# Optimization experiments

Hardware: AMD Instinct MI355X
Metric: run time of the kernel (lower is better)

The kernel has to match this reference:

```python
import jax, jax.numpy as jnp
import numpy as np

N = 4096            # tokens (dim 0 of x)
LATENT = 1024       # latent_vector_size
H = 16              # num_heads
DK = 64             # key_dim
DV = 64             # val_dim
MHK = H * DK        # 1024, width of q and k blocks


def setup_inputs() -> dict:
    key = jax.random.key(0)
    ks = jax.random.split(key, 5)
    return {
        "x": jax.random.normal(ks[0], (N, LATENT), dtype=jnp.float32),
        "w_qkv": jax.random.normal(ks[1], (LATENT, H * (2 * DK + DV)), dtype=jnp.float32) * (1.0 / np.sqrt(LATENT)),
        "b_qkv": jax.random.normal(ks[2], (H * (2 * DK + DV),), dtype=jnp.float32) * 0.01,
        "w_out": jax.random.normal(ks[3], (H * DV, LATENT), dtype=jnp.float32) * (1.0 / np.sqrt(H * DV)),
        "b_out": jax.random.normal(ks[4], (LATENT,), dtype=jnp.float32) * 0.01,
    }


def reference(x, w_qkv, b_qkv, w_out, b_out):
    # qkv projection: [N, H*(2*Dk+Dv)]
    qkv = x @ w_qkv + b_qkv
    # NOTE: the original module does NOT split into heads; q/k/v are the
    # concatenated head dims and a single [N, N] score matrix is formed,
    # scaled by sqrt(key_dim) (per-head dim), not sqrt(H*key_dim).
    q = qkv[:, :MHK]                 # [N, H*Dk]
    k = qkv[:, MHK:2 * MHK]          # [N, H*Dk]
    v = qkv[:, 2 * MHK:]             # [N, H*Dv]
    scores = (q @ k.T) * (1.0 / jnp.sqrt(jnp.float32(DK)))  # [N, N]
    attn = jax.nn.softmax(scores, axis=-1)
    out = attn @ v                   # [N, H*Dv]
    return out @ w_out + b_out       # [N, LATENT]
```

## Files before the change

### kernel.cpp

```cpp
#include <hip/hip_runtime.h>
#include <hip/hip_fp16.h>


typedef _Float16 half_t;
typedef _Float16 half8 __attribute__((ext_vector_type(8)));
typedef _Float16 half4 __attribute__((ext_vector_type(4)));
typedef float f32x4 __attribute__((ext_vector_type(4)));

static constexpr int N_TOK = 4096;
static constexpr int LATENT = 1024;
static constexpr int QKVN = 3072;

#define DEVI __device__ __forceinline__
#define BAR() __builtin_amdgcn_s_barrier()
#define PRIO(x) __builtin_amdgcn_s_setprio(x)
#define VMCNT(n) asm volatile("s_waitcnt vmcnt(" #n ")" ::: "memory")

DEVI void gld_lds16(const half_t* g, half_t* l) {
  __builtin_amdgcn_global_load_lds(
      (const __attribute__((address_space(1))) void*)g,
      (__attribute__((address_space(3))) void*)l,
      16, 0, 0);
}

DEVI f32x4 MFMA(half8 a, half8 b, f32x4 c) {
  return __builtin_amdgcn_mfma_f32_16x16x32_f16(a, b, c, 0, 0, 0);
}


DEVI void stageH(const half_t* __restrict__ g, int ld, half_t* lbase, int tid) {
#pragma unroll
  for (int i = 0; i < 2; ++i) {
    int c = tid + i * 512;
    int r = c >> 2;
    int k8 = ((c & 3) ^ ((r >> 1) & 3)) * 8;
    gld_lds16(g + (size_t)r * ld + k8, lbase + c * 8);
  }
}

template <int MODE>
__launch_bounds__(512, 2)
__global__ void gemm8h(const half_t* __restrict__ A, int lda,
                       const half_t* __restrict__ B, int ldb,
                       void* __restrict__ Cout, int ldc,
                       const float* __restrict__ bias, int K) {
  __shared__ half_t Alds[2][2][256 * 32];
  __shared__ half_t Blds[2][2][256 * 32];

  const int tid = threadIdx.x;
  const int lane = tid & 63;
  const int wid = tid >> 6;

  const int nx = gridDim.x;
  const int nwg = nx * gridDim.y;
  const int bid = blockIdx.y * nx + blockIdx.x;
  const int cpx = nwg >> 3;
  const int swz = (bid & 7) * cpx + (bid >> 3);
  const int rowBlk = (swz / nx) * 256;
  const int colBlk = (swz % nx) * 256;

  const int wr = (wid >> 2) * 128;
  const int wc = (wid & 3) * 64;
  const int fr = lane & 15;
  const int fs = lane >> 4;

  const int kOff = blockIdx.z * K;
  const half_t* Ag = A + (size_t)rowBlk * lda + kOff;
  const half_t* Bg = B + (size_t)colBlk * ldb + kOff;

  f32x4 acc[8][4] = {};
  const int NT = K >> 6;

  stageH(Ag, lda, Alds[0][0], tid);
  stageH(Bg, ldb, Blds[0][0], tid);
  stageH(Ag + 32, lda, Alds[0][1], tid);
  stageH(Bg + 32, ldb, Blds[0][1], tid);
  VMCNT(4);
  BAR();

  for (int kt = 0; kt < NT; ++kt) {
    const int b = kt & 1;
    const bool st = (kt + 1 < NT);
    const half_t* AgN = Ag + (kt + 1) * 64;
    const half_t* BgN = Bg + (kt + 1) * 64;

    half8 af[8], bf[4];
#pragma unroll
    for (int kh = 0; kh < 2; ++kh) {
      const half_t* Ac = Alds[b][kh];
      const half_t* Bc = Blds[b][kh];
#pragma unroll
      for (int m = 0; m < 8; ++m) {
        int row = wr + m * 16 + fr;
        af[m] = *(const half8*)(Ac + row * 32 + ((fs ^ ((row >> 1) & 3)) * 8));
      }
#pragma unroll
      for (int n = 0; n < 4; ++n) {
        int row = wc + n * 16 + fr;
        bf[n] = *(const half8*)(Bc + row * 32 + ((fs ^ ((row >> 1) & 3)) * 8));
      }
      if (st) {
        stageH(AgN + kh * 32, lda, Alds[b ^ 1][kh], tid);
        stageH(BgN + kh * 32, ldb, Blds[b ^ 1][kh], tid);
      }
      BAR();
      PRIO(1);
#pragma unroll
      for (int m = 0; m < 8; ++m)
#pragma unroll
        for (int n = 0; n < 4; ++n)
          acc[m][n] = MFMA(af[m], bf[n], acc[m][n]);
      PRIO(0);
      if (st) VMCNT(4);
      else if (kh == 0) VMCNT(0);
      BAR();
    }
  }

  const size_t zoff = (MODE == 2) ? (size_t)blockIdx.z * N_TOK * ldc : 0;
#pragma unroll
  for (int m = 0; m < 8; ++m) {
#pragma unroll
    for (int n = 0; n < 4; ++n) {
#pragma unroll
      for (int j = 0; j < 4; ++j) {
        int row = rowBlk + wr + m * 16 + (lane >> 4) * 4 + j;
        int col = colBlk + wc + n * 16 + fr;
        float v = acc[m][n][j];
        if (MODE == 0) {
          v += bias[col];
          if (col < 1024) v *= 0.125f;
          ((half_t*)Cout)[(size_t)row * ldc + col] = (half_t)v;
        } else if (MODE == 1) {
          ((half_t*)Cout)[(size_t)row * ldc + col] = (half_t)v;
        } else {
          ((half_t*)Cout)[zoff + (size_t)row * ldc + col] = (half_t)v;
        }
      }
    }
  }
}

DEVI void stage32p(const half_t* __restrict__ g, int ld, half_t* lbase, int tid) {
#pragma unroll
  for (int c = tid; c < 128 * 4; c += 256) {
    int r = c >> 2;
    int k8 = ((c & 3) ^ ((r >> 1) & 3)) * 8;
    gld_lds16(g + (size_t)r * ld + k8, lbase + c * 8);
  }
}

__launch_bounds__(256, 2)
__global__ void vwt_softmax(const half_t* __restrict__ wo,
                            const half_t* __restrict__ v,
                            half_t* __restrict__ vwT,
                            const half_t* __restrict__ S,
                            half_t* __restrict__ P) {
  __shared__ __align__(16) char smem[32768];
  const int bid = blockIdx.x;
  const int tid = threadIdx.x;

  if (bid < 256) {
    constexpr int BM = 128, BN = 128, MF = 4, NF = 4;
    half_t* At = (half_t*)smem;
    half_t* Bt = At + 2 * BM * 32;

    const int lane = tid & 63;
    const int wid = tid >> 6;
    const int swz = (bid & 7) * 32 + (bid >> 3);
    const int rowBlk = (swz >> 5) * BM;
    const int colBlk = (swz & 31) * BN;

    const int wr = (wid >> 1) * (BM / 2);
    const int wc = (wid & 1) * (BN / 2);
    const int fr = lane & 15;
    const int fs = lane >> 4;

    const half_t* Ag = wo + (size_t)rowBlk * LATENT;
    const half_t* Bg = v + (size_t)colBlk * QKVN;

    f32x4 acc[MF][NF] = {};
    const int NT = LATENT >> 5;
    stage32p(Ag, LATENT, At, tid);
    stage32p(Bg, QKVN, Bt, tid);
    __syncthreads();

    int cur = 0;
    for (int t = 0; t < NT; ++t) {
      if (t + 1 < NT) {
        stage32p(Ag + (t + 1) * 32, LATENT, At + (cur ^ 1) * BM * 32, tid);
        stage32p(Bg + (t + 1) * 32, QKVN, Bt + (cur ^ 1) * BN * 32, tid);
      }
      const half_t* Ac = At + cur * BM * 32;
      const half_t* Bc = Bt + cur * BN * 32;
      half8 af[MF], bf[NF];
#pragma unroll
      for (int m = 0; m < MF; ++m) {
        int row = wr + m * 16 + fr;
        af[m] = *(const half8*)(Ac + row * 32 + ((fs ^ ((row >> 1) & 3)) * 8));
      }
#pragma unroll
      for (int n = 0; n < NF; ++n) {
        int row = wc + n * 16 + fr;
        bf[n] = *(const half8*)(Bc + row * 32 + ((fs ^ ((row >> 1) & 3)) * 8));
      }
#pragma unroll
      for (int m = 0; m < MF; ++m)
#pragma unroll
        for (int n = 0; n < NF; ++n)
          acc[m][n] = MFMA(af[m], bf[n], acc[m][n]);
      __syncthreads();
      cur ^= 1;
    }

#pragma unroll
    for (int m = 0; m < MF; ++m)
#pragma unroll
      for (int n = 0; n < NF; ++n)
#pragma unroll
        for (int j = 0; j < 4; ++j) {
          int row = rowBlk + wr + m * 16 + (lane >> 4) * 4 + j;
          int col = colBlk + wc + n * 16 + fr;
          vwT[(size_t)row * N_TOK + col] = (half_t)acc[m][n][j];
        }
  } else {
    const int row = bid - 256;
    float* redm = (float*)smem;
    float* reds = redm + 4;
    const half8* s8 = (const half8*)(S + (size_t)row * N_TOK);

    half8 vv[2];
    float lmax = -1e30f;
#pragma unroll
    for (int i = 0; i < 2; ++i) {
      vv[i] = s8[tid + i * 256];
#pragma unroll
      for (int j = 0; j < 8; ++j) lmax = fmaxf(lmax, (float)vv[i][j]);
    }
#pragma unroll
    for (int off = 32; off; off >>= 1) lmax = fmaxf(lmax, __shfl_xor(lmax, off));
    if ((tid & 63) == 0) redm[tid >> 6] = lmax;
    __syncthreads();
    lmax = fmaxf(fmaxf(redm[0], redm[1]), fmaxf(redm[2], redm[3]));

    float e[16];
    float lsum = 0.f;
#pragma unroll
    for (int i = 0; i < 2; ++i)
#pragma unroll
      for (int j = 0; j < 8; ++j) {
        float ev = __expf((float)vv[i][j] - lmax);
        e[i * 8 + j] = ev;
        lsum += ev;
      }
#pragma unroll
    for (int off = 32; off; off >>= 1) lsum += __shfl_xor(lsum, off);
    if ((tid & 63) == 0) reds[tid >> 6] = lsum;
    __syncthreads();
    float inv = 1.f / (reds[0] + reds[1] + reds[2] + reds[3]);

    half8* p8 = (half8*)(P + (size_t)row * N_TOK);
#pragma unroll
    for (int i = 0; i < 2; ++i) {
      half8 h;
#pragma unroll
      for (int j = 0; j < 8; ++j) h[j] = (half_t)(e[i * 8 + j] * inv);
      p8[tid + i * 256] = h;
    }
  }
}

__launch_bounds__(256)
__global__ void reduce_bias4(const half_t* __restrict__ p, const float* __restrict__ bias,
                             float* __restrict__ out) {
  int i = blockIdx.x * 256 + threadIdx.x;
  const size_t stride8 = (size_t)N_TOK * LATENT / 8;
  half8 a = ((const half8*)p)[i];
  half8 b = ((const half8*)p)[i + stride8];
  half8 c = ((const half8*)p)[i + 2 * stride8];
  half8 d = ((const half8*)p)[i + 3 * stride8];
  float4 e0 = ((const float4*)bias)[(i & 127) * 2];
  float4 e1 = ((const float4*)bias)[(i & 127) * 2 + 1];
  float r[8];
#pragma unroll
  for (int j = 0; j < 8; ++j)
    r[j] = (float)a[j] + (float)b[j] + (float)c[j] + (float)d[j];
  float4 o0, o1;
  o0.x = r[0] + e0.x; o0.y = r[1] + e0.y; o0.z = r[2] + e0.z; o0.w = r[3] + e0.w;
  o1.x = r[4] + e1.x; o1.y = r[5] + e1.y; o1.z = r[6] + e1.z; o1.w = r[7] + e1.w;
  ((float4*)out)[i * 2] = o0;
  ((float4*)out)[i * 2 + 1] = o1;
}

DEVI void tr32(const float* __restrict__ in, int ldin,
               half_t* __restrict__ out, int ldout,
               int cb, int rb, int tid, float (*tile)[33]) {
  const int tx = tid & 31;
  const int ty = tid >> 5;
#pragma unroll
  for (int i = ty; i < 32; i += 8)
    tile[i][tx] = in[(size_t)(rb + i) * ldin + cb + tx];
  __syncthreads();
#pragma unroll
  for (int i = ty; i < 32; i += 8)
    out[(size_t)(cb + i) * ldout + rb + tx] = (half_t)tile[tx][i];
}

__launch_bounds__(256)
__global__ void preamble(const float* __restrict__ x, half_t* __restrict__ xb,
                         const float* __restrict__ wq, half_t* __restrict__ wqT,
                         const float* __restrict__ wo, half_t* __restrict__ woT) {
  __shared__ float tile[32][33];
  const int bid = blockIdx.x;
  const int tid = threadIdx.x;
  if (bid < 4096) {
    int i = bid * 256 + tid;
    float4 v = ((const float4*)x)[i];
    half4 h;
    h[0] = (half_t)v.x; h[1] = (half_t)v.y; h[2] = (half_t)v.z; h[3] = (half_t)v.w;
    ((half4*)xb)[i] = h;
  } else if (bid < 7168) {
    int l = bid - 4096;
    tr32(wq, QKVN, wqT, LATENT, (l % 96) * 32, (l / 96) * 32, tid, tile);
  } else {
    int l = bid - 7168;
    tr32(wo, LATENT, woT, LATENT, (l & 31) * 32, (l >> 5) * 32, tid, tile);
  }
}

extern "C" void kernel_launch(void* const* d_in, const int* in_sizes, int n_in,
                              void* d_out, int out_size, void* d_ws, size_t ws_size,
                              hipStream_t stream) {
  const float* x = (const float*)d_in[0];
  const float* w_qkv = (const float*)d_in[1];
  const float* b_qkv = (const float*)d_in[2];
  const float* w_out = (const float*)d_in[3];
  const float* b_out = (const float*)d_in[4];
  float* out = (float*)d_out;

  char* ws = (char*)d_ws;
  half_t* xb    = (half_t*)(ws);
  half_t* wqkvT = (half_t*)(ws + ((size_t)8 << 20));
  half_t* qkv   = (half_t*)(ws + ((size_t)14 << 20));
  half_t* S     = (half_t*)(ws + ((size_t)46 << 20));
  half_t* P     = (half_t*)(ws + ((size_t)78 << 20));
  half_t* vwT   = (half_t*)(ws + ((size_t)118 << 20));
  half_t* woutT = (half_t*)(ws + ((size_t)126 << 20));
  half_t* parts = (half_t*)(ws + ((size_t)14 << 20));

  preamble<<<8192, 256, 0, stream>>>(x, xb, w_qkv, wqkvT, w_out, woutT);
  gemm8h<0><<<dim3(QKVN / 256, N_TOK / 256), 512, 0, stream>>>(
      xb, LATENT, wqkvT, LATENT, qkv, QKVN, b_qkv, LATENT);
  gemm8h<1><<<dim3(N_TOK / 256, N_TOK / 256), 512, 0, stream>>>(
      qkv, QKVN, qkv + LATENT, QKVN, S, N_TOK, nullptr, LATENT);
  vwt_softmax<<<256 + N_TOK, 256, 0, stream>>>(
      woutT, qkv + 2 * LATENT, vwT, S, P);
  gemm8h<2><<<dim3(LATENT / 256, N_TOK / 256, 4), 512, 0, stream>>>(
      P, N_TOK, vwT, N_TOK, parts, LATENT, nullptr, 1024);
  reduce_bias4<<<(N_TOK * LATENT) / (256 * 8), 256, 0, stream>>>(parts, b_out, out);
}
```

Measured before the change: 155.7 us.

## Replace split-K output GEMM and reduction with a single full-K fused-bias GEMM

The final P·vwT projection ran as a 4-way split-K GEMM writing fp16 partials, then a separate kernel summed them and added the bias. It is now a dedicated 128x128-tile GEMM over the full K=4096 that adds the bias and writes fp32 output directly. This removes the partial-sum write/read traffic and one kernel launch, at the cost of smaller tiles with lower data reuse and a longer serial K loop per workgroup. The redundant barrier between the LDS fragment loads and the MFMA block is also dropped in both GEMMs.

```diff
diff --git a/kernel.cpp b/kernel.cpp
--- a/kernel.cpp
+++ b/kernel.cpp
@@ -32,6 +32,16 @@
 #pragma unroll
   for (int i = 0; i < 2; ++i) {
     int c = tid + i * 512;
+    int r = c >> 2;
+    int k8 = ((c & 3) ^ ((r >> 1) & 3)) * 8;
+    gld_lds16(g + (size_t)r * ld + k8, lbase + c * 8);
+  }
+}
+
+DEVI void stageH128(const half_t* __restrict__ g, int ld, half_t* lbase, int tid) {
+#pragma unroll
+  for (int i = 0; i < 2; ++i) {
+    int c = tid + i * 256;
     int r = c >> 2;
     int k8 = ((c & 3) ^ ((r >> 1) & 3)) * 8;
     gld_lds16(g + (size_t)r * ld + k8, lbase + c * 8);
@@ -64,9 +74,8 @@
   const int fr = lane & 15;
   const int fs = lane >> 4;
 
-  const int kOff = blockIdx.z * K;
-  const half_t* Ag = A + (size_t)rowBlk * lda + kOff;
-  const half_t* Bg = B + (size_t)colBlk * ldb + kOff;
+  const half_t* Ag = A + (size_t)rowBlk * lda;
+  const half_t* Bg = B + (size_t)colBlk * ldb;
 
   f32x4 acc[8][4] = {};
   const int NT = K >> 6;
@@ -103,7 +112,6 @@
         stageH(AgN + kh * 32, lda, Alds[b ^ 1][kh], tid);
         stageH(BgN + kh * 32, ldb, Blds[b ^ 1][kh], tid);
       }
-      BAR();
       PRIO(1);
 #pragma unroll
       for (int m = 0; m < 8; ++m)
@@ -117,7 +125,6 @@
     }
   }
 
-  const size_t zoff = (MODE == 2) ? (size_t)blockIdx.z * N_TOK * ldc : 0;
 #pragma unroll
   for (int m = 0; m < 8; ++m) {
 #pragma unroll
@@ -131,11 +138,100 @@
           v += bias[col];
           if (col < 1024) v *= 0.125f;
           ((half_t*)Cout)[(size_t)row * ldc + col] = (half_t)v;
-        } else if (MODE == 1) {
+        } else {
           ((half_t*)Cout)[(size_t)row * ldc + col] = (half_t)v;
-        } else {
-          ((half_t*)Cout)[zoff + (size_t)row * ldc + col] = (half_t)v;
         }
+      }
+    }
+  }
+}
+
+__launch_bounds__(256, 2)
+__global__ void gemmF(const half_t* __restrict__ A,
+                      const half_t* __restrict__ B,
+                      const float* __restrict__ bias,
+                      float* __restrict__ out) {
+  __shared__ half_t Alds[2][2][128 * 32];
+  __shared__ half_t Blds[2][2][128 * 32];
+
+  const int tid = threadIdx.x;
+  const int lane = tid & 63;
+  const int wid = tid >> 6;
+  constexpr int K = 4096;
+
+  const int nx = gridDim.x;
+  const int nwg = nx * gridDim.y;
+  const int bid = blockIdx.y * nx + blockIdx.x;
+  const int cpx = nwg >> 3;
+  const int swz = (bid & 7) * cpx + (bid >> 3);
+  const int rowBlk = (swz / nx) * 128;
+  const int colBlk = (swz % nx) * 128;
+
+  const int wr = (wid >> 1) * 64;
+  const int wc = (wid & 1) * 64;
+  const int fr = lane & 15;
+  const int fs = lane >> 4;
+
+  const half_t* Ag = A + (size_t)rowBlk * N_TOK;
+  const half_t* Bg = B + (size_t)colBlk * N_TOK;
+
+  f32x4 acc[4][4] = {};
+  const int NT = K >> 6;
+
+  stageH128(Ag, N_TOK, Alds[0][0], tid);
+  stageH128(Bg, N_TOK, Blds[0][0], tid);
+  stageH128(Ag + 32, N_TOK, Alds[0][1], tid);
+  stageH128(Bg + 32, N_TOK, Blds[0][1], tid);
+  VMCNT(4);
+  BAR();
+
+  for (int kt = 0; kt < NT; ++kt) {
+    const int b = kt & 1;
+    const bool st = (kt + 1 < NT);
+    const half_t* AgN = Ag + (kt + 1) * 64;
+    const half_t* BgN = Bg + (kt + 1) * 64;
+
+    half8 af[4], bf[4];
+#pragma unroll
+    for (int kh = 0; kh < 2; ++kh) {
+      const half_t* Ac = Alds[b][kh];
+      const half_t* Bc = Blds[b][kh];
+#pragma unroll
+      for (int m = 0; m < 4; ++m) {
+        int row = wr + m * 16 + fr;
+        af[m] = *(const half8*)(Ac + row * 32 + ((fs ^ ((row >> 1) & 3)) * 8));
+      }
+#pragma unroll
+      for (int n = 0; n < 4; ++n) {
+        int row = wc + n * 16 + fr;
+        bf[n] = *(const half8*)(Bc + row * 32 + ((fs ^ ((row >> 1) & 3)) * 8));
+      }
+      if (st) {
+        stageH128(AgN + kh * 32, N_TOK, Alds[b ^ 1][kh], tid);
+        stageH128(BgN + kh * 32, N_TOK, Blds[b ^ 1][kh], tid);
+      }
+      PRIO(1);
+#pragma unroll
+      for (int m = 0; m < 4; ++m)
+#pragma unroll
+        for (int n = 0; n < 4; ++n)
+          acc[m][n] = MFMA(af[m], bf[n], acc[m][n]);
+      PRIO(0);
+      if (st) VMCNT(4);
+      else if (kh == 0) VMCNT(0);
+      BAR();
+    }
+  }
+
+#pragma unroll
+  for (int m = 0; m < 4; ++m) {
+#pragma unroll
+    for (int n = 0; n < 4; ++n) {
+#pragma unroll
+      for (int j = 0; j < 4; ++j) {
+        int row = rowBlk + wr + m * 16 + (lane >> 4) * 4 + j;
+        int col = colBlk + wc + n * 16 + fr;
+        out[(size_t)row * LATENT + col] = acc[m][n][j] + bias[col];
       }
     }
   }
@@ -268,28 +364,6 @@
       p8[tid + i * 256] = h;
     }
   }
-}
-
-__launch_bounds__(256)
-__global__ void reduce_bias4(const half_t* __restrict__ p, const float* __restrict__ bias,
-                             float* __restrict__ out) {
-  int i = blockIdx.x * 256 + threadIdx.x;
-  const size_t stride8 = (size_t)N_TOK * LATENT / 8;
-  half8 a = ((const half8*)p)[i];
-  half8 b = ((const half8*)p)[i + stride8];
-  half8 c = ((const half8*)p)[i + 2 * stride8];
-  half8 d = ((const half8*)p)[i + 3 * stride8];
-  float4 e0 = ((const float4*)bias)[(i & 127) * 2];
-  float4 e1 = ((const float4*)bias)[(i & 127) * 2 + 1];
-  float r[8];
-#pragma unroll
-  for (int j = 0; j < 8; ++j)
-    r[j] = (float)a[j] + (float)b[j] + (float)c[j] + (float)d[j];
-  float4 o0, o1;
-  o0.x = r[0] + e0.x; o0.y = r[1] + e0.y; o0.z = r[2] + e0.z; o0.w = r[3] + e0.w;
-  o1.x = r[4] + e1.x; o1.y = r[5] + e1.y; o1.z = r[6] + e1.z; o1.w = r[7] + e1.w;
-  ((float4*)out)[i * 2] = o0;
-  ((float4*)out)[i * 2 + 1] = o1;
 }
 
 DEVI void tr32(const float* __restrict__ in, int ldin,
@@ -346,7 +420,6 @@
   half_t* P     = (half_t*)(ws + ((size_t)78 << 20));
   half_t* vwT   = (half_t*)(ws + ((size_t)118 << 20));
   half_t* woutT = (half_t*)(ws + ((size_t)126 << 20));
-  half_t* parts = (half_t*)(ws + ((size_t)14 << 20));
 
   preamble<<<8192, 256, 0, stream>>>(x, xb, w_qkv, wqkvT, w_out, woutT);
   gemm8h<0><<<dim3(QKVN / 256, N_TOK / 256), 512, 0, stream>>>(
@@ -355,7 +428,6 @@
       qkv, QKVN, qkv + LATENT, QKVN, S, N_TOK, nullptr, LATENT);
   vwt_softmax<<<256 + N_TOK, 256, 0, stream>>>(
       woutT, qkv + 2 * LATENT, vwT, S, P);
-  gemm8h<2><<<dim3(LATENT / 256, N_TOK / 256, 4), 512, 0, stream>>>(
-      P, N_TOK, vwT, N_TOK, parts, LATENT, nullptr, 1024);
-  reduce_bias4<<<(N_TOK * LATENT) / (256 * 8), 256, 0, stream>>>(parts, b_out, out);
-}
+  gemmF<<<dim3(LATENT / 128, N_TOK / 128), 256, 0, stream>>>(
+      P, vwT, b_out, out);
+}
```

New measurement: 161.1 us. 3.5% more time.
